# Kernel optimization log

Hardware: AMD Instinct MI355X
Metric: run time of the kernel (lower is better)

Reference implementation:

```python
import jax, jax.numpy as jnp
import numpy as np

EPS = 1e-5

def _linear(x, w, b):
    # torch nn.Linear convention: w is [out, in]
    return jnp.einsum('...i,oi->...o', x, w) + b

def _l2_normalize(x, axis=-1):
    n = jnp.sqrt(jnp.sum(x * x, axis=axis, keepdims=True))
    return x / jnp.maximum(n, 1e-12)

def _online_softmax_scan(sim):
    # sim: [B, H, L]. Running max m_t and running sum s_t = sum_{i<=t} exp(sim_i - m_t)
    def combine(a, b):
        ma, sa = a
        mb, sb = b
        m = jnp.maximum(ma, mb)
        s = sa * jnp.exp(ma - m) + sb * jnp.exp(mb - m)
        return m, s
    m_scan, s_scan = jax.lax.associative_scan(combine, (sim, jnp.ones_like(sim)), axis=2)
    return m_scan, s_scan


def setup_inputs() -> dict:
    key = jax.random.key(0)
    ks = jax.random.split(key, 8)
    B, L, D = 2, 2048, 256
    H, h = 8, 32
    s = 1.0 / np.sqrt(D)
    inp = {
        'x': jax.random.normal(ks[0], (B, L, D), jnp.float32),
        'wq_w': jax.random.normal(ks[1], (D, D), jnp.float32) * s,
        'wq_b': jnp.zeros((D,), jnp.float32),
        'wk_w': jax.random.normal(ks[2], (D, D), jnp.float32) * s,
        'wk_b': jnp.zeros((D,), jnp.float32),
        'wv_w': jax.random.normal(ks[3], (D, D), jnp.float32) * s,
        'wv_b': jnp.zeros((D,), jnp.float32),
        'wo_w': jax.random.normal(ks[4], (D, D), jnp.float32) * s,
        'wo_b': jnp.zeros((D,), jnp.float32),
        'wg_w': jax.random.normal(ks[5], (1, h * h), jnp.float32) * (1.0 / np.sqrt(h * h)),
        'wg_b': jnp.zeros((1,), jnp.float32),
        'kv_norm_scale': jnp.ones((1, H, 1, h, h), jnp.float32),
        'qk_norm_scale': jnp.full((1, H, 1), 1.0 / np.sqrt(h), jnp.float32),
    }
    return inp


def reference(x, wq_w, wq_b, wk_w, wk_b, wv_w, wv_b, wo_w, wo_b,
              wg_w, wg_b, kv_norm_scale, qk_norm_scale):
    B, L, D = x.shape
    H, h = kv_norm_scale.shape[1], kv_norm_scale.shape[3]

    q = _linear(x, wq_w, wq_b).reshape(B, L, H, h).transpose(0, 2, 1, 3)  # bhld
    k = _linear(x, wk_w, wk_b).reshape(B, L, H, h).transpose(0, 2, 1, 3)
    v = _linear(x, wv_w, wv_b).reshape(B, L, H, h).transpose(0, 2, 1, 3)

    sim = jnp.einsum('bhld,bhld->bhl', q, k) * qk_norm_scale  # [B,H,L]

    k = _l2_normalize(k)
    v = _l2_normalize(v)

    # outer-product KV state per position: [B,H,L,h,h]
    Z = jnp.einsum('bhld,bhle->bhlde', v, k) * kv_norm_scale

    # gating: squared ReLU of linear over flattened h*h features
    gate_inputs = Z.reshape(B, H, L, h * h)
    gates_logits = jnp.einsum('bhli,oi->bhlo', gate_inputs, wg_w) + wg_b  # [B,H,L,1]
    gates = jnp.square(jax.nn.relu(gates_logits)) + EPS
    gates = gates[..., None]  # [B,H,L,1,1]
    gated_Z = gates * Z

    # associative scans along L
    m_scan, s_scan = _online_softmax_scan(sim)        # [B,H,L]
    Z_scan = jnp.cumsum(gated_Z, axis=2)              # [B,H,L,h,h]
    g_scan = jnp.cumsum(gates, axis=2)                # [B,H,L,1,1]

    softmax_weights = (jnp.exp(sim - m_scan) / (s_scan + EPS))[..., None, None]
    gated_weights = Z_scan / (g_scan + EPS)
    attn_weights = gated_weights * (1.0 + jax.nn.silu(softmax_weights))

    ctxt = jnp.einsum('bhld,bhlde->bhle', q, attn_weights)
    ctxt = ctxt.transpose(0, 2, 1, 3).reshape(B, L, D)
    return _linear(ctxt, wo_w, wo_b)
```

## Files before the change

### kernel.cpp

```cpp
#include <hip/hip_runtime.h>
#include <math.h>

#define EPSV 1e-5f

static constexpr int Ls = 2048, Hh = 8;
static constexpr int NCH = 64, T = 32;

typedef unsigned short u16;
using frag  = __attribute__((ext_vector_type(8))) short;
using f32x4 = __attribute__((ext_vector_type(4))) float;

__device__ __forceinline__ void split_bf16(float v, u16& hi, u16& lo) {
    const unsigned u = __float_as_uint(v);
    hi = (u16)(u >> 16);
    const float hf = __uint_as_float((unsigned)hi << 16);
    lo = (u16)(__float_as_uint(v - hf) >> 16);
}

__device__ __forceinline__ unsigned pk2(u16 a, u16 b) {
    return (unsigned)a | ((unsigned)b << 16);
}

__device__ __forceinline__ void split8(const float4& a, const float4& b,
                                       uint4& hi, uint4& lo) {
    u16 h[8], l[8];
    const float f[8] = {a.x, a.y, a.z, a.w, b.x, b.y, b.z, b.w};
#pragma unroll
    for (int i = 0; i < 8; ++i) split_bf16(f[i], h[i], l[i]);
    hi = make_uint4(pk2(h[0], h[1]), pk2(h[2], h[3]), pk2(h[4], h[5]), pk2(h[6], h[7]));
    lo = make_uint4(pk2(l[0], l[1]), pk2(l[2], l[3]), pk2(l[4], l[5]), pk2(l[6], l[7]));
}

__global__ __launch_bounds__(256) void qkv_fused(
    const float* __restrict__ x,
    const float* __restrict__ wq, const float* __restrict__ wk, const float* __restrict__ wv,
    const float* __restrict__ bq, const float* __restrict__ bk, const float* __restrict__ bv,
    const float* __restrict__ wg_w, const float* __restrict__ wg_b,
    const float* __restrict__ kvs, const float* __restrict__ qks,
    float* __restrict__ qh, float* __restrict__ kh, float* __restrict__ vh,
    float* __restrict__ simG, float* __restrict__ gG,
    float* __restrict__ ZcT, float* __restrict__ mT, float* __restrict__ sT,
    float* __restrict__ gTt)
{
    constexpr int LDK = 40;
    constexpr int LDT = 66;
    __shared__ __align__(16) float smemf[3 * 64 * LDT];
    __shared__ float wkS[2][1024];
    __shared__ float lsim[2][64], lg2[2][64];

    u16* As_hi = (u16*)smemf;
    u16* As_lo = As_hi + 2560;
    u16* Wst   = As_lo + 2560;
    float* Qt = smemf;
    float* Kt = Qt + 64 * LDT;
    float* Vt = Kt + 64 * LDT;

    const int tid = threadIdx.x;
    const int mt = blockIdx.x, nt = blockIdx.y;
    const int m0 = mt * 64, ncol0 = nt * 64;
    const int bidx = m0 >> 11, lg = m0 & (Ls - 1);
    const int wave = tid >> 6, lane = tid & 63;
    const int l15 = lane & 15, quad = lane >> 4;
    const int srow = tid >> 2, sk = (tid & 3) * 8;

    for (int i = tid; i < 2048; i += 256) {
        const int h = i >> 10, de = i & 1023;
        wkS[h][de] = wg_w[de] * kvs[(nt * 2 + h) * 1024 + de];
    }

    const float* Wsrc[3] = {wq, wk, wv};
    f32x4 acc[3][4] = {};

    for (int k0 = 0; k0 < 256; k0 += 32) {
        const float4 a0 = *(const float4*)&x[(size_t)(m0 + srow) * 256 + k0 + sk];
        const float4 a1 = *(const float4*)&x[(size_t)(m0 + srow) * 256 + k0 + sk + 4];
        float4 w0[3], w1[3];
#pragma unroll
        for (int w = 0; w < 3; ++w) {
            w0[w] = *(const float4*)&Wsrc[w][(size_t)(ncol0 + srow) * 256 + k0 + sk];
            w1[w] = *(const float4*)&Wsrc[w][(size_t)(ncol0 + srow) * 256 + k0 + sk + 4];
        }
        __syncthreads();
        {
            uint4 hi, lo;
            split8(a0, a1, hi, lo);
            *(uint4*)&As_hi[srow * LDK + sk] = hi;
            *(uint4*)&As_lo[srow * LDK + sk] = lo;
#pragma unroll
            for (int w = 0; w < 3; ++w) {
                split8(w0[w], w1[w], hi, lo);
                *(uint4*)&Wst[w * 5120 + srow * LDK + sk] = hi;
                *(uint4*)&Wst[w * 5120 + 2560 + srow * LDK + sk] = lo;
            }
        }
        __syncthreads();

        const frag ah = *(const frag*)&As_hi[(wave * 16 + l15) * LDK + quad * 8];
        const frag al = *(const frag*)&As_lo[(wave * 16 + l15) * LDK + quad * 8];
#pragma unroll
        for (int w = 0; w < 3; ++w)
#pragma unroll
            for (int cf = 0; cf < 4; ++cf) {
                const u16* bp = &Wst[w * 5120 + (cf * 16 + l15) * LDK + quad * 8];
                const frag bh = *(const frag*)bp;
                const frag bl = *(const frag*)(bp + 2560);
                acc[w][cf] = __builtin_amdgcn_mfma_f32_16x16x32_bf16(ah, bh, acc[w][cf], 0, 0, 0);
                acc[w][cf] = __builtin_amdgcn_mfma_f32_16x16x32_bf16(ah, bl, acc[w][cf], 0, 0, 0);
                acc[w][cf] = __builtin_amdgcn_mfma_f32_16x16x32_bf16(al, bh, acc[w][cf], 0, 0, 0);
            }
    }
    __syncthreads();

    {
        float* tiles[3] = {Qt, Kt, Vt};
        const float* biases[3] = {bq, bk, bv};
#pragma unroll
        for (int w = 0; w < 3; ++w)
#pragma unroll
            for (int cf = 0; cf < 4; ++cf) {
                const int col = cf * 16 + l15;
                const float bias = biases[w][ncol0 + col];
#pragma unroll
                for (int r = 0; r < 4; ++r) {
                    const int m = wave * 16 + quad * 4 + r;
                    tiles[w][m * LDT + col] = acc[w][cf][r] + bias;
                }
            }
    }
    __syncthreads();

    if (tid < 128) {
        const int h = tid >> 6, l = tid & 63;
        const int cb = h * 32;
        float ksum = 0.f, vsum = 0.f, qk = 0.f;
#pragma unroll 8
        for (int e = 0; e < 32; ++e) {
            const float kv = Kt[l * LDT + cb + e];
            const float vv = Vt[l * LDT + cb + e];
            const float qv = Qt[l * LDT + cb + e];
            ksum = fmaf(kv, kv, ksum);
            vsum = fmaf(vv, vv, vsum);
            qk = fmaf(qv, kv, qk);
        }
        const float kscale = 1.f / fmaxf(sqrtf(ksum), 1e-12f);
        const float vscale = 1.f / fmaxf(sqrtf(vsum), 1e-12f);
#pragma unroll 8
        for (int e = 0; e < 32; ++e) {
            Kt[l * LDT + cb + e] *= kscale;
            Vt[l * LDT + cb + e] *= vscale;
        }
        const float sim = qk * qks[nt * 2 + h];
        lsim[h][l] = sim;
        simG[(size_t)(bidx * 8 + nt * 2 + h) * Ls + lg + l] = sim;
    }
    __syncthreads();

    {
        const float* tl[3] = {Qt, Kt, Vt};
        float* gl[3] = {qh, kh, vh};
#pragma unroll
        for (int arr = 0; arr < 3; ++arr)
#pragma unroll
            for (int it = 0; it < 8; ++it) {
                const int idx = it * 512 + tid * 2;
                const int h = idx >> 11, rem = idx & 2047;
                const int l = rem >> 5, e = rem & 31;
                float2 v;
                v.x = tl[arr][l * LDT + h * 32 + e];
                v.y = tl[arr][l * LDT + h * 32 + e + 1];
                *(float2*)&gl[arr][(size_t)(bidx * 8 + nt * 2 + h) * 65536 +
                                   (size_t)(lg + l) * 32 + e] = v;
            }
    }

    {
        const int task = tid >> 1, half = tid & 1;
        const int h = task >> 6, l = task & 63;
        float vreg[32];
#pragma unroll 8
        for (int d = 0; d < 32; ++d) vreg[d] = Vt[l * LDT + h * 32 + d];
        float u = 0.f;
        const int e0 = half * 16;
#pragma unroll 4
        for (int e = e0; e < e0 + 16; ++e) {
            float s = 0.f;
#pragma unroll 8
            for (int d = 0; d < 32; ++d)
                s = fmaf(vreg[d], wkS[h][d * 32 + e], s);
            u = fmaf(s, Kt[l * LDT + h * 32 + e], u);
        }
        u += __shfl_xor(u, 1);
        if (half == 0) {
            const float r = fmaxf(u + wg_b[0], 0.f);
            const float g = r * r + EPSV;
            lg2[h][l] = g;
            gG[(size_t)(bidx * 8 + nt * 2 + h) * Ls + lg + l] = g;
        }
    }
    __syncthreads();

    {
        const int d = tid >> 3, e0 = (tid & 7) * 4;
#pragma unroll
        for (int h = 0; h < 2; ++h)
#pragma unroll
            for (int cc = 0; cc < 2; ++cc) {
                float z0 = 0.f, z1 = 0.f, z2 = 0.f, z3 = 0.f;
#pragma unroll 8
                for (int l = 0; l < 32; ++l) {
                    const int lr = cc * 32 + l;
                    const float gv = lg2[h][lr] * Vt[lr * LDT + h * 32 + d];
                    z0 = fmaf(gv, Kt[lr * LDT + h * 32 + e0 + 0], z0);
                    z1 = fmaf(gv, Kt[lr * LDT + h * 32 + e0 + 1], z1);
                    z2 = fmaf(gv, Kt[lr * LDT + h * 32 + e0 + 2], z2);
                    z3 = fmaf(gv, Kt[lr * LDT + h * 32 + e0 + 3], z3);
                }
                const int bhg = bidx * 8 + nt * 2 + h;
                const int cg = (lg >> 5) + cc;
                float4 zv; zv.x = z0; zv.y = z1; zv.z = z2; zv.w = z3;
                *(float4*)&ZcT[((size_t)bhg * NCH + cg) * 1024 + d * 32 + e0] = zv;
            }
    }

    {
        const int h = wave >> 1, cc = wave & 1;
        if (lane < 32) {
            const int lr = cc * 32 + lane;
            float m = lsim[h][lr], s = 1.f, g = lg2[h][lr];
#pragma unroll
            for (int off = 16; off; off >>= 1) {
                const float mo = __shfl_xor(m, off);
                const float so = __shfl_xor(s, off);
                const float mn = fmaxf(m, mo);
                s = s * __expf(m - mn) + so * __expf(mo - mn);
                m = mn;
                g += __shfl_xor(g, off);
            }
            if (lane == 0) {
                const int bhg = bidx * 8 + nt * 2 + h;
                const int cg = (lg >> 5) + cc;
                mT[bhg * NCH + cg] = m;
                sT[bhg * NCH + cg] = s;
                gTt[bhg * NCH + cg] = g;
            }
        }
    }
}

__global__ __launch_bounds__(256) void prefix_kernel(
    float* __restrict__ Zc, float* __restrict__ mT, float* __restrict__ sT,
    float* __restrict__ gTt,
    const float* __restrict__ kvs, float* __restrict__ aW, float* __restrict__ bW,
    int* __restrict__ flagW)
{
    const int bh = blockIdx.x, seg = blockIdx.y;
    const int tid = threadIdx.x;
    const int el = seg * 256 + tid;
    float* Zb = Zc + (size_t)bh * NCH * 1024 + el;

    float run = 0.f;
#pragma unroll
    for (int cb = 0; cb < NCH; cb += 8) {
        float v[8];
#pragma unroll
        for (int i = 0; i < 8; ++i) v[i] = Zb[(size_t)(cb + i) * 1024];
#pragma unroll
        for (int i = 0; i < 8; ++i) {
            const float t = v[i];
            Zb[(size_t)(cb + i) * 1024] = run;
            run += t;
        }
    }

    if (seg == 0 && tid < 64) {
        float m = mT[bh * NCH + tid], s = sT[bh * NCH + tid], g = gTt[bh * NCH + tid];
#pragma unroll
        for (int off = 1; off < 64; off <<= 1) {
            const float mo = __shfl_up(m, off);
            const float so = __shfl_up(s, off);
            const float go = __shfl_up(g, off);
            if (tid >= off) {
                const float mn = fmaxf(m, mo);
                s = s * __expf(m - mn) + so * __expf(mo - mn);
                m = mn;
                g += go;
            }
        }
        float me = __shfl_up(m, 1), se = __shfl_up(s, 1), ge = __shfl_up(g, 1);
        if (tid == 0) { me = -1e30f; se = 0.f; ge = 0.f; }
        mT[bh * NCH + tid] = me;
        sT[bh * NCH + tid] = se;
        gTt[bh * NCH + tid] = ge;
    }

    if (bh == 0 && seg == 3) {
        const int h = tid >> 5, e = tid & 31;
        const float* K = kvs + h * 1024;
        const float k00 = K[0];
        int ok = (k00 != 0.0f);
        for (int d = 0; d < 32; ++d) {
            const float lhs = K[d * 32 + e] * k00;
            const float rhs = K[d * 32] * K[e];
            const float diff = fabsf(lhs - rhs);
            if (diff > 1e-6f * fmaxf(fmaxf(fabsf(lhs), fabsf(rhs)), 1e-20f)) ok = 0;
        }
        aW[h * 32 + e] = K[e * 32];
        bW[h * 32 + e] = (k00 != 0.0f) ? K[e] / k00 : 0.f;
        const int allok = __syncthreads_and(ok);
        if (tid == 0) flagW[0] = allok;
    }
}

__global__ __launch_bounds__(1024) void chunk_out_kernel(
    const float* __restrict__ qh, const float* __restrict__ knG, const float* __restrict__ vnG,
    const float* __restrict__ simG, const float* __restrict__ gG,
    const float* __restrict__ kvs,
    const float* __restrict__ ZcP, const float* __restrict__ mP,
    const float* __restrict__ sP, const float* __restrict__ gP,
    const float* __restrict__ aW, const float* __restrict__ bW,
    const int* __restrict__ flagW,
    u16* __restrict__ chi, u16* __restrict__ clo)
{
    __shared__ float qa[1024], knb[1024], zp[1024], lkvs[1024];
    __shared__ float vnT[32 * 33], sW[32 * 33];
    __shared__ float la[32], lb[32], lg[T], lsim[T], lwgt[T];
    const int tid = threadIdx.x;
    const int c = blockIdx.x, bh = blockIdx.y, h = bh & 7, b = bh >> 3;
    const int l = tid >> 5, lane = tid & 31;
    const size_t base = ((size_t)bh * Ls + c * T) * 32;
    const int flag = flagW[0];

    const float qv = qh[base + tid];
    const float knv = knG[base + tid];
    const float vnv = vnG[base + tid];
    vnT[lane * 33 + l] = vnv;
    zp[tid] = ZcP[((size_t)bh * NCH + c) * 1024 + tid];
    if (!flag) lkvs[tid] = kvs[h * 1024 + tid];
    if (tid < 32) {
        la[tid] = aW[h * 32 + tid];
        lb[tid] = bW[h * 32 + tid];
        lg[tid] = gG[bh * Ls + c * T + tid];
        lsim[tid] = simG[bh * Ls + c * T + tid];
    }
    __syncthreads();

    qa[tid] = flag ? qv * la[lane] : qv;
    knb[tid] = flag ? knv * lb[lane] : knv;
    if (tid < 32) {
        float m = lsim[tid], s = 1.f, g = lg[tid];
#pragma unroll
        for (int off = 1; off < 32; off <<= 1) {
            const float mo = __shfl_up(m, off);
            const float so = __shfl_up(s, off);
            const float go = __shfl_up(g, off);
            if (tid >= off) {
                const float mn = fmaxf(m, mo);
                s = s * __expf(m - mn) + so * __expf(mo - mn);
                m = mn;
                g += go;
            }
        }
        const float mp = mP[bh * NCH + c];
        const float sp = sP[bh * NCH + c];
        const float gp = gP[bh * NCH + c];
        const float mn = fmaxf(mp, m);
        s = sp * __expf(mp - mn) + s * __expf(m - mn);
        m = mn;
        g += gp;
        const float sw = __expf(lsim[tid] - m) / (s + EPSV);
        const float sig = 1.f / (1.f + __expf(-sw));
        lwgt[tid] = (1.f + sw * sig) / (g + EPSV);
    }
    __syncthreads();

    float y;
    if (flag) {
        float s = 0.f, y0 = 0.f;
        const float4* qa4 = (const float4*)&qa[l * 32];
#pragma unroll
        for (int d4 = 0; d4 < 8; ++d4) {
            const float4 q4 = qa4[d4];
            const int d = d4 * 4;
            s = fmaf(q4.x, vnT[(d + 0) * 33 + lane], s);
            s = fmaf(q4.y, vnT[(d + 1) * 33 + lane], s);
            s = fmaf(q4.z, vnT[(d + 2) * 33 + lane], s);
            s = fmaf(q4.w, vnT[(d + 3) * 33 + lane], s);
            y0 = fmaf(q4.x, zp[(d + 0) * 32 + lane], y0);
            y0 = fmaf(q4.y, zp[(d + 1) * 32 + lane], y0);
            y0 = fmaf(q4.z, zp[(d + 2) * 32 + lane], y0);
            y0 = fmaf(q4.w, zp[(d + 3) * 32 + lane], y0);
        }
        sW[l * 33 + lane] = (lane <= l) ? lg[lane] * s : 0.f;
        __syncthreads();
        y = y0 * lb[lane];
#pragma unroll 8
        for (int j = 0; j < 32; ++j)
            y = fmaf(sW[l * 33 + j], knb[j * 32 + lane], y);
        y *= lwgt[l];
    } else {
        float qe[32];
#pragma unroll
        for (int d = 0; d < 32; ++d)
            qe[d] = qa[l * 32 + d] * lkvs[d * 32 + lane];
        y = 0.f;
#pragma unroll
        for (int d = 0; d < 32; ++d)
            y = fmaf(qe[d], zp[d * 32 + lane], y);
        for (int j = 0; j < 32; ++j) {
            float s = 0.f;
#pragma unroll
            for (int d = 0; d < 32; ++d)
                s = fmaf(qe[d], vnT[d * 33 + j], s);
            if (j <= l) y = fmaf(lg[j] * s, knb[j * 32 + lane], y);
        }
        y *= lwgt[l];
    }
    u16 hi, lo;
    split_bf16(y, hi, lo);
    const size_t oidx = ((size_t)(b * Ls + c * T + l)) * 256 + h * 32 + lane;
    chi[oidx] = hi;
    clo[oidx] = lo;
}

__global__ __launch_bounds__(256) void out_gemm(
    const u16* __restrict__ Ahi, const u16* __restrict__ Alo,
    const float* __restrict__ wo, const float* __restrict__ bo,
    float* __restrict__ out)
{
    constexpr int LDK = 40;
    __shared__ __align__(16) u16 As_hi[64 * LDK];
    __shared__ __align__(16) u16 As_lo[64 * LDK];
    __shared__ __align__(16) u16 Ws_hi[64 * LDK];
    __shared__ __align__(16) u16 Ws_lo[64 * LDK];

    const int tid = threadIdx.x;
    const int mt = blockIdx.x, nt = blockIdx.y;
    const int m0 = mt * 64, ncol0 = nt * 64;
    const int wave = tid >> 6, lane = tid & 63;
    const int l15 = lane & 15, quad = lane >> 4;
    const int srow = tid >> 2, sk = (tid & 3) * 8;

    f32x4 acc[4] = {};

    for (int k0 = 0; k0 < 256; k0 += 32) {
        const uint4 ah = *(const uint4*)&Ahi[(size_t)(m0 + srow) * 256 + k0 + sk];
        const uint4 al = *(const uint4*)&Alo[(size_t)(m0 + srow) * 256 + k0 + sk];
        const float4 w0 = *(const float4*)&wo[(size_t)(ncol0 + srow) * 256 + k0 + sk];
        const float4 w1 = *(const float4*)&wo[(size_t)(ncol0 + srow) * 256 + k0 + sk + 4];
        __syncthreads();
        uint4 whi, wlo;
        split8(w0, w1, whi, wlo);
        *(uint4*)&As_hi[srow * LDK + sk] = ah;
        *(uint4*)&As_lo[srow * LDK + sk] = al;
        *(uint4*)&Ws_hi[srow * LDK + sk] = whi;
        *(uint4*)&Ws_lo[srow * LDK + sk] = wlo;
        __syncthreads();

        const frag fah = *(const frag*)&As_hi[(wave * 16 + l15) * LDK + quad * 8];
        const frag fal = *(const frag*)&As_lo[(wave * 16 + l15) * LDK + quad * 8];
#pragma unroll
        for (int cf = 0; cf < 4; ++cf) {
            const frag fbh = *(const frag*)&Ws_hi[(cf * 16 + l15) * LDK + quad * 8];
            const frag fbl = *(const frag*)&Ws_lo[(cf * 16 + l15) * LDK + quad * 8];
            acc[cf] = __builtin_amdgcn_mfma_f32_16x16x32_bf16(fah, fbh, acc[cf], 0, 0, 0);
            acc[cf] = __builtin_amdgcn_mfma_f32_16x16x32_bf16(fah, fbl, acc[cf], 0, 0, 0);
            acc[cf] = __builtin_amdgcn_mfma_f32_16x16x32_bf16(fal, fbh, acc[cf], 0, 0, 0);
        }
    }

#pragma unroll
    for (int cf = 0; cf < 4; ++cf) {
        const int o = ncol0 + cf * 16 + l15;
        const float bias = bo[o];
#pragma unroll
        for (int r = 0; r < 4; ++r) {
            const int rm = m0 + wave * 16 + quad * 4 + r;
            out[(size_t)rm * 256 + o] = acc[cf][r] + bias;
        }
    }
}

extern "C" void kernel_launch(void* const* d_in, const int* in_sizes, int n_in,
                              void* d_out, int out_size, void* d_ws, size_t ws_size,
                              hipStream_t stream) {
    const float* x    = (const float*)d_in[0];
    const float* wq_w = (const float*)d_in[1];
    const float* wq_b = (const float*)d_in[2];
    const float* wk_w = (const float*)d_in[3];
    const float* wk_b = (const float*)d_in[4];
    const float* wv_w = (const float*)d_in[5];
    const float* wv_b = (const float*)d_in[6];
    const float* wo_w = (const float*)d_in[7];
    const float* wo_b = (const float*)d_in[8];
    const float* wg_w = (const float*)d_in[9];
    const float* wg_b = (const float*)d_in[10];
    const float* kvs  = (const float*)d_in[11];
    const float* qks  = (const float*)d_in[12];
    float* out = (float*)d_out;

    u16* chi = (u16*)d_ws;
    u16* clo = chi + 1048576;
    float* qh   = (float*)(clo + 1048576);
    float* kh   = qh + 1048576;
    float* vh   = kh + 1048576;
    float* ZcT  = vh + 1048576;
    float* simG = ZcT + 1048576;
    float* gG   = simG + 32768;
    float* mT   = gG + 32768;
    float* sT   = mT + 1024;
    float* gTt  = sT + 1024;
    float* aW   = gTt + 1024;
    float* bW   = aW + 256;
    int* flagW  = (int*)(bW + 256);

    qkv_fused<<<dim3(64, 4), 256, 0, stream>>>(
        x, wq_w, wk_w, wv_w, wq_b, wk_b, wv_b, wg_w, wg_b, kvs, qks,
        qh, kh, vh, simG, gG, ZcT, mT, sT, gTt);
    prefix_kernel<<<dim3(16, 4), 256, 0, stream>>>(
        ZcT, mT, sT, gTt, kvs, aW, bW, flagW);
    chunk_out_kernel<<<dim3(NCH, 16), 1024, 0, stream>>>(
        qh, kh, vh, simG, gG, kvs, ZcT, mT, sT, gTt, aW, bW, flagW, chi, clo);
    out_gemm<<<dim3(64, 4), 256, 0, stream>>>(
        chi, clo, wo_w, wo_b, out);
}
```

Measured before the change: 145.9 us.

## Halve row tile to 32 in QKV and output GEMMs to double grid size

Both the fused QKV kernel and the output GEMM now process 32 rows per block instead of 64, which doubles the grid from 256 to 512 blocks. Waves are re-mapped to a 2x2 layout over row and column fragments, and the per-row norm and gate work is split across 4 threads with shuffle reductions. The aim is to fill more of the device's compute units in these small GEMMs. In exchange, weight tiles are loaded and split twice as often in total, and the per-chunk ZcT and scan statistics are now written once per block.

```diff
diff --git a/kernel.cpp b/kernel.cpp
--- a/kernel.cpp
+++ b/kernel.cpp
@@ -44,24 +44,26 @@
 {
     constexpr int LDK = 40;
     constexpr int LDT = 66;
-    __shared__ __align__(16) float smemf[3 * 64 * LDT];
+    __shared__ __align__(16) float smemf[8960];
     __shared__ float wkS[2][1024];
-    __shared__ float lsim[2][64], lg2[2][64];
+    __shared__ float lsim[2][32], lg2[2][32];
 
     u16* As_hi = (u16*)smemf;
-    u16* As_lo = As_hi + 2560;
-    u16* Wst   = As_lo + 2560;
+    u16* As_lo = As_hi + 1280;
+    u16* Wst   = As_lo + 1280;
     float* Qt = smemf;
-    float* Kt = Qt + 64 * LDT;
-    float* Vt = Kt + 64 * LDT;
+    float* Kt = Qt + 32 * LDT;
+    float* Vt = Kt + 32 * LDT;
 
     const int tid = threadIdx.x;
     const int mt = blockIdx.x, nt = blockIdx.y;
-    const int m0 = mt * 64, ncol0 = nt * 64;
+    const int m0 = mt * 32, ncol0 = nt * 64;
     const int bidx = m0 >> 11, lg = m0 & (Ls - 1);
+    const int cg = lg >> 5;
     const int wave = tid >> 6, lane = tid & 63;
     const int l15 = lane & 15, quad = lane >> 4;
     const int srow = tid >> 2, sk = (tid & 3) * 8;
+    const int rf = wave & 1, cfp = wave >> 1;
 
     for (int i = tid; i < 2048; i += 256) {
         const int h = i >> 10, de = i & 1023;
@@ -69,11 +71,14 @@
     }
 
     const float* Wsrc[3] = {wq, wk, wv};
-    f32x4 acc[3][4] = {};
+    f32x4 acc[3][2] = {};
 
     for (int k0 = 0; k0 < 256; k0 += 32) {
-        const float4 a0 = *(const float4*)&x[(size_t)(m0 + srow) * 256 + k0 + sk];
-        const float4 a1 = *(const float4*)&x[(size_t)(m0 + srow) * 256 + k0 + sk + 4];
+        float4 a0, a1;
+        if (tid < 128) {
+            a0 = *(const float4*)&x[(size_t)(m0 + srow) * 256 + k0 + sk];
+            a1 = *(const float4*)&x[(size_t)(m0 + srow) * 256 + k0 + sk + 4];
+        }
         float4 w0[3], w1[3];
 #pragma unroll
         for (int w = 0; w < 3; ++w) {
@@ -83,9 +88,11 @@
         __syncthreads();
         {
             uint4 hi, lo;
-            split8(a0, a1, hi, lo);
-            *(uint4*)&As_hi[srow * LDK + sk] = hi;
-            *(uint4*)&As_lo[srow * LDK + sk] = lo;
+            if (tid < 128) {
+                split8(a0, a1, hi, lo);
+                *(uint4*)&As_hi[srow * LDK + sk] = hi;
+                *(uint4*)&As_lo[srow * LDK + sk] = lo;
+            }
 #pragma unroll
             for (int w = 0; w < 3; ++w) {
                 split8(w0[w], w1[w], hi, lo);
@@ -95,13 +102,13 @@
         }
         __syncthreads();
 
-        const frag ah = *(const frag*)&As_hi[(wave * 16 + l15) * LDK + quad * 8];
-        const frag al = *(const frag*)&As_lo[(wave * 16 + l15) * LDK + quad * 8];
+        const frag ah = *(const frag*)&As_hi[(rf * 16 + l15) * LDK + quad * 8];
+        const frag al = *(const frag*)&As_lo[(rf * 16 + l15) * LDK + quad * 8];
 #pragma unroll
         for (int w = 0; w < 3; ++w)
 #pragma unroll
-            for (int cf = 0; cf < 4; ++cf) {
-                const u16* bp = &Wst[w * 5120 + (cf * 16 + l15) * LDK + quad * 8];
+            for (int cf = 0; cf < 2; ++cf) {
+                const u16* bp = &Wst[w * 5120 + ((cfp * 2 + cf) * 16 + l15) * LDK + quad * 8];
                 const frag bh = *(const frag*)bp;
                 const frag bl = *(const frag*)(bp + 2560);
                 acc[w][cf] = __builtin_amdgcn_mfma_f32_16x16x32_bf16(ah, bh, acc[w][cf], 0, 0, 0);
@@ -117,24 +124,25 @@
 #pragma unroll
         for (int w = 0; w < 3; ++w)
 #pragma unroll
-            for (int cf = 0; cf < 4; ++cf) {
-                const int col = cf * 16 + l15;
+            for (int cf = 0; cf < 2; ++cf) {
+                const int col = (cfp * 2 + cf) * 16 + l15;
                 const float bias = biases[w][ncol0 + col];
 #pragma unroll
                 for (int r = 0; r < 4; ++r) {
-                    const int m = wave * 16 + quad * 4 + r;
+                    const int m = rf * 16 + quad * 4 + r;
                     tiles[w][m * LDT + col] = acc[w][cf][r] + bias;
                 }
             }
     }
     __syncthreads();
 
-    if (tid < 128) {
-        const int h = tid >> 6, l = tid & 63;
-        const int cb = h * 32;
+    {
+        const int task = tid >> 2, sub = tid & 3;
+        const int h = task >> 5, l = task & 31;
+        const int cb = h * 32, e0 = sub * 8;
         float ksum = 0.f, vsum = 0.f, qk = 0.f;
-#pragma unroll 8
-        for (int e = 0; e < 32; ++e) {
+#pragma unroll
+        for (int e = e0; e < e0 + 8; ++e) {
             const float kv = Kt[l * LDT + cb + e];
             const float vv = Vt[l * LDT + cb + e];
             const float qv = Qt[l * LDT + cb + e];
@@ -142,16 +150,21 @@
             vsum = fmaf(vv, vv, vsum);
             qk = fmaf(qv, kv, qk);
         }
+        ksum += __shfl_xor(ksum, 1); ksum += __shfl_xor(ksum, 2);
+        vsum += __shfl_xor(vsum, 1); vsum += __shfl_xor(vsum, 2);
+        qk   += __shfl_xor(qk, 1);   qk   += __shfl_xor(qk, 2);
         const float kscale = 1.f / fmaxf(sqrtf(ksum), 1e-12f);
         const float vscale = 1.f / fmaxf(sqrtf(vsum), 1e-12f);
-#pragma unroll 8
-        for (int e = 0; e < 32; ++e) {
+#pragma unroll
+        for (int e = e0; e < e0 + 8; ++e) {
             Kt[l * LDT + cb + e] *= kscale;
             Vt[l * LDT + cb + e] *= vscale;
         }
-        const float sim = qk * qks[nt * 2 + h];
-        lsim[h][l] = sim;
-        simG[(size_t)(bidx * 8 + nt * 2 + h) * Ls + lg + l] = sim;
+        if (sub == 0) {
+            const float sim = qk * qks[nt * 2 + h];
+            lsim[h][l] = sim;
+            simG[(size_t)(bidx * 8 + nt * 2 + h) * Ls + lg + l] = sim;
+        }
     }
     __syncthreads();
 
@@ -161,10 +174,10 @@
 #pragma unroll
         for (int arr = 0; arr < 3; ++arr)
 #pragma unroll
-            for (int it = 0; it < 8; ++it) {
+            for (int it = 0; it < 4; ++it) {
                 const int idx = it * 512 + tid * 2;
-                const int h = idx >> 11, rem = idx & 2047;
-                const int l = rem >> 5, e = rem & 31;
+                const int l = idx >> 6, col = idx & 63;
+                const int h = col >> 5, e = col & 31;
                 float2 v;
                 v.x = tl[arr][l * LDT + h * 32 + e];
                 v.y = tl[arr][l * LDT + h * 32 + e + 1];
@@ -174,15 +187,15 @@
     }
 
     {
-        const int task = tid >> 1, half = tid & 1;
-        const int h = task >> 6, l = task & 63;
+        const int task = tid >> 2, sub = tid & 3;
+        const int h = task >> 5, l = task & 31;
         float vreg[32];
 #pragma unroll 8
         for (int d = 0; d < 32; ++d) vreg[d] = Vt[l * LDT + h * 32 + d];
         float u = 0.f;
-        const int e0 = half * 16;
-#pragma unroll 4
-        for (int e = e0; e < e0 + 16; ++e) {
+        const int e0 = sub * 8;
+#pragma unroll
+        for (int e = e0; e < e0 + 8; ++e) {
             float s = 0.f;
 #pragma unroll 8
             for (int d = 0; d < 32; ++d)
@@ -190,7 +203,8 @@
             u = fmaf(s, Kt[l * LDT + h * 32 + e], u);
         }
         u += __shfl_xor(u, 1);
-        if (half == 0) {
+        u += __shfl_xor(u, 2);
+        if (sub == 0) {
             const float r = fmaxf(u + wg_b[0], 0.f);
             const float g = r * r + EPSV;
             lg2[h][l] = g;
@@ -202,47 +216,39 @@
     {
         const int d = tid >> 3, e0 = (tid & 7) * 4;
 #pragma unroll
-        for (int h = 0; h < 2; ++h)
-#pragma unroll
-            for (int cc = 0; cc < 2; ++cc) {
-                float z0 = 0.f, z1 = 0.f, z2 = 0.f, z3 = 0.f;
+        for (int h = 0; h < 2; ++h) {
+            float z0 = 0.f, z1 = 0.f, z2 = 0.f, z3 = 0.f;
 #pragma unroll 8
-                for (int l = 0; l < 32; ++l) {
-                    const int lr = cc * 32 + l;
-                    const float gv = lg2[h][lr] * Vt[lr * LDT + h * 32 + d];
-                    z0 = fmaf(gv, Kt[lr * LDT + h * 32 + e0 + 0], z0);
-                    z1 = fmaf(gv, Kt[lr * LDT + h * 32 + e0 + 1], z1);
-                    z2 = fmaf(gv, Kt[lr * LDT + h * 32 + e0 + 2], z2);
-                    z3 = fmaf(gv, Kt[lr * LDT + h * 32 + e0 + 3], z3);
-                }
-                const int bhg = bidx * 8 + nt * 2 + h;
-                const int cg = (lg >> 5) + cc;
-                float4 zv; zv.x = z0; zv.y = z1; zv.z = z2; zv.w = z3;
-                *(float4*)&ZcT[((size_t)bhg * NCH + cg) * 1024 + d * 32 + e0] = zv;
-            }
-    }
-
-    {
-        const int h = wave >> 1, cc = wave & 1;
-        if (lane < 32) {
-            const int lr = cc * 32 + lane;
-            float m = lsim[h][lr], s = 1.f, g = lg2[h][lr];
-#pragma unroll
-            for (int off = 16; off; off >>= 1) {
-                const float mo = __shfl_xor(m, off);
-                const float so = __shfl_xor(s, off);
-                const float mn = fmaxf(m, mo);
-                s = s * __expf(m - mn) + so * __expf(mo - mn);
-                m = mn;
-                g += __shfl_xor(g, off);
-            }
-            if (lane == 0) {
-                const int bhg = bidx * 8 + nt * 2 + h;
-                const int cg = (lg >> 5) + cc;
-                mT[bhg * NCH + cg] = m;
-                sT[bhg * NCH + cg] = s;
-                gTt[bhg * NCH + cg] = g;
-            }
+            for (int l = 0; l < 32; ++l) {
+                const float gv = lg2[h][l] * Vt[l * LDT + h * 32 + d];
+                z0 = fmaf(gv, Kt[l * LDT + h * 32 + e0 + 0], z0);
+                z1 = fmaf(gv, Kt[l * LDT + h * 32 + e0 + 1], z1);
+                z2 = fmaf(gv, Kt[l * LDT + h * 32 + e0 + 2], z2);
+                z3 = fmaf(gv, Kt[l * LDT + h * 32 + e0 + 3], z3);
+            }
+            const int bhg = bidx * 8 + nt * 2 + h;
+            float4 zv; zv.x = z0; zv.y = z1; zv.z = z2; zv.w = z3;
+            *(float4*)&ZcT[((size_t)bhg * NCH + cg) * 1024 + d * 32 + e0] = zv;
+        }
+    }
+
+    if (wave < 2 && lane < 32) {
+        const int h = wave;
+        float m = lsim[h][lane], s = 1.f, g = lg2[h][lane];
+#pragma unroll
+        for (int off = 16; off; off >>= 1) {
+            const float mo = __shfl_xor(m, off);
+            const float so = __shfl_xor(s, off);
+            const float mn = fmaxf(m, mo);
+            s = s * __expf(m - mn) + so * __expf(mo - mn);
+            m = mn;
+            g += __shfl_xor(g, off);
+        }
+        if (lane == 0) {
+            const int bhg = bidx * 8 + nt * 2 + h;
+            mT[bhg * NCH + cg] = m;
+            sT[bhg * NCH + cg] = s;
+            gTt[bhg * NCH + cg] = g;
         }
     }
 }
@@ -428,40 +434,46 @@
     float* __restrict__ out)
 {
     constexpr int LDK = 40;
-    __shared__ __align__(16) u16 As_hi[64 * LDK];
-    __shared__ __align__(16) u16 As_lo[64 * LDK];
+    __shared__ __align__(16) u16 As_hi[32 * LDK];
+    __shared__ __align__(16) u16 As_lo[32 * LDK];
     __shared__ __align__(16) u16 Ws_hi[64 * LDK];
     __shared__ __align__(16) u16 Ws_lo[64 * LDK];
 
     const int tid = threadIdx.x;
     const int mt = blockIdx.x, nt = blockIdx.y;
-    const int m0 = mt * 64, ncol0 = nt * 64;
+    const int m0 = mt * 32, ncol0 = nt * 64;
     const int wave = tid >> 6, lane = tid & 63;
     const int l15 = lane & 15, quad = lane >> 4;
     const int srow = tid >> 2, sk = (tid & 3) * 8;
-
-    f32x4 acc[4] = {};
+    const int rf = wave & 1, cfp = wave >> 1;
+
+    f32x4 acc[2] = {};
 
     for (int k0 = 0; k0 < 256; k0 += 32) {
-        const uint4 ah = *(const uint4*)&Ahi[(size_t)(m0 + srow) * 256 + k0 + sk];
-        const uint4 al = *(const uint4*)&Alo[(size_t)(m0 + srow) * 256 + k0 + sk];
+        uint4 ah, al;
+        if (tid < 128) {
+            ah = *(const uint4*)&Ahi[(size_t)(m0 + srow) * 256 + k0 + sk];
+            al = *(const uint4*)&Alo[(size_t)(m0 + srow) * 256 + k0 + sk];
+        }
         const float4 w0 = *(const float4*)&wo[(size_t)(ncol0 + srow) * 256 + k0 + sk];
         const float4 w1 = *(const float4*)&wo[(size_t)(ncol0 + srow) * 256 + k0 + sk + 4];
         __syncthreads();
         uint4 whi, wlo;
         split8(w0, w1, whi, wlo);
-        *(uint4*)&As_hi[srow * LDK + sk] = ah;
-        *(uint4*)&As_lo[srow * LDK + sk] = al;
+        if (tid < 128) {
+            *(uint4*)&As_hi[srow * LDK + sk] = ah;
+            *(uint4*)&As_lo[srow * LDK + sk] = al;
+        }
         *(uint4*)&Ws_hi[srow * LDK + sk] = whi;
         *(uint4*)&Ws_lo[srow * LDK + sk] = wlo;
         __syncthreads();
 
-        const frag fah = *(const frag*)&As_hi[(wave * 16 + l15) * LDK + quad * 8];
-        const frag fal = *(const frag*)&As_lo[(wave * 16 + l15) * LDK + quad * 8];
-#pragma unroll
-        for (int cf = 0; cf < 4; ++cf) {
-            const frag fbh = *(const frag*)&Ws_hi[(cf * 16 + l15) * LDK + quad * 8];
-            const frag fbl = *(const frag*)&Ws_lo[(cf * 16 + l15) * LDK + quad * 8];
+        const frag fah = *(const frag*)&As_hi[(rf * 16 + l15) * LDK + quad * 8];
+        const frag fal = *(const frag*)&As_lo[(rf * 16 + l15) * LDK + quad * 8];
+#pragma unroll
+        for (int cf = 0; cf < 2; ++cf) {
+            const frag fbh = *(const frag*)&Ws_hi[((cfp * 2 + cf) * 16 + l15) * LDK + quad * 8];
+            const frag fbl = *(const frag*)&Ws_lo[((cfp * 2 + cf) * 16 + l15) * LDK + quad * 8];
             acc[cf] = __builtin_amdgcn_mfma_f32_16x16x32_bf16(fah, fbh, acc[cf], 0, 0, 0);
             acc[cf] = __builtin_amdgcn_mfma_f32_16x16x32_bf16(fah, fbl, acc[cf], 0, 0, 0);
             acc[cf] = __builtin_amdgcn_mfma_f32_16x16x32_bf16(fal, fbh, acc[cf], 0, 0, 0);
@@ -469,12 +481,12 @@
     }
 
 #pragma unroll
-    for (int cf = 0; cf < 4; ++cf) {
-        const int o = ncol0 + cf * 16 + l15;
+    for (int cf = 0; cf < 2; ++cf) {
+        const int o = ncol0 + (cfp * 2 + cf) * 16 + l15;
         const float bias = bo[o];
 #pragma unroll
         for (int r = 0; r < 4; ++r) {
-            const int rm = m0 + wave * 16 + quad * 4 + r;
+            const int rm = m0 + rf * 16 + quad * 4 + r;
             out[(size_t)rm * 256 + o] = acc[cf][r] + bias;
         }
     }
@@ -513,13 +525,13 @@
     float* bW   = aW + 256;
     int* flagW  = (int*)(bW + 256);
 
-    qkv_fused<<<dim3(64, 4), 256, 0, stream>>>(
+    qkv_fused<<<dim3(128, 4), 256, 0, stream>>>(
         x, wq_w, wk_w, wv_w, wq_b, wk_b, wv_b, wg_w, wg_b, kvs, qks,
         qh, kh, vh, simG, gG, ZcT, mT, sT, gTt);
     prefix_kernel<<<dim3(16, 4), 256, 0, stream>>>(
         ZcT, mT, sT, gTt, kvs, aW, bW, flagW);
     chunk_out_kernel<<<dim3(NCH, 16), 1024, 0, stream>>>(
         qh, kh, vh, simG, gG, kvs, ZcT, mT, sT, gTt, aW, bW, flagW, chi, clo);
-    out_gemm<<<dim3(64, 4), 256, 0, stream>>>(
+    out_gemm<<<dim3(128, 4), 256, 0, stream>>>(
         chi, clo, wo_w, wo_b, out);
 }
```

Measured after the change: 135.5 us. 1.08x faster.
